# Optimization experiments

Hardware: AMD Instinct MI355X
Metric: run time of the kernel (lower is better)

Reference implementation:

```python
import jax, jax.numpy as jnp
import numpy as np

B, S, D, F = 8, 2048, 256, 8

def setup_inputs() -> dict:
    key = jax.random.key(0)
    ks = jax.random.split(key, 7)
    hidden_states = jax.random.normal(ks[0], (B, S, D), dtype=jnp.float32)
    # flat indices into zero-prepended [1 + B*S, D] token table; 0 = padding row
    select_idx = jax.random.randint(ks[1], (B, S, F), 0, B * S + 1, dtype=jnp.int32)
    word_mask = jax.random.randint(ks[2], (B, S), 0, 2, dtype=jnp.int32)
    W1 = jax.random.normal(ks[3], (D, D), dtype=jnp.float32) * (1.0 / np.sqrt(D))
    b1 = jax.random.normal(ks[4], (D,), dtype=jnp.float32) * 0.02
    w2 = jax.random.normal(ks[5], (D,), dtype=jnp.float32) * (1.0 / np.sqrt(D))
    b2 = jax.random.normal(ks[6], (1,), dtype=jnp.float32) * 0.02
    return {"hidden_states": hidden_states, "select_idx": select_idx,
            "word_mask": word_mask, "W1": W1, "b1": b1, "w2": w2, "b2": b2}

def reference(hidden_states, select_idx, word_mask, W1, b1, w2, b2):
    b, s, d = hidden_states.shape
    h = jnp.tanh(hidden_states.reshape(-1, d) @ W1.T + b1)          # [B*S, D]
    h = jnp.concatenate([jnp.zeros((1, d), h.dtype), h], axis=0)    # zero padding row at index 0
    g = h[select_idx.reshape(-1)]                                    # gather: [B*S*F, D]
    g = g.reshape(b * s, -1, d).max(axis=1)                          # AdaptiveMaxPool1d(1) over word occurrences
    scores = (g @ w2 + b2[0]).reshape(b, s)                          # w2 linear -> [B, S]
    neg = -10000.0 * (1.0 - word_mask.astype(jnp.float32))
    return scores.astype(jnp.float32) + neg
```

## Files before the change

### kernel.cpp

```cpp
#include <hip/hip_runtime.h>
#include <hip/hip_bf16.h>
#include <math.h>

#define BB 8
#define SS 2048
#define DD 256
#define FF 8
#define NTOK (BB*SS)

typedef __bf16 bf16x8 __attribute__((ext_vector_type(8)));
typedef float  f32x4  __attribute__((ext_vector_type(4)));
typedef float  f32x2  __attribute__((ext_vector_type(2)));

#define BM 128
#define BN 64
#define BK 32
#define NSTEP (DD/BK)
#define XS 40

__device__ __forceinline__ float fast_tanh(float x) {
    float e = __expf(2.0f * x);
    return 1.0f - 2.0f * __builtin_amdgcn_rcpf(e + 1.0f);
}

__device__ __forceinline__ unsigned pack2_bf16(float a, float b) {
    return (__float_as_uint(a) >> 16) | (__float_as_uint(b) & 0xFFFF0000u);
}

__device__ __forceinline__ unsigned char f32_to_fp8(float v) {
    return (unsigned char)(__builtin_amdgcn_cvt_pk_fp8_f32(v, v, 0, false) & 0xFF);
}

__global__ __launch_bounds__(512, 4) void gemm_tanh_kernel(
    const float* __restrict__ x, const float* __restrict__ W1,
    const float* __restrict__ b1, unsigned char* __restrict__ table)
{
    __shared__ __align__(16) unsigned short xs[2][BM * XS];
    __shared__ __align__(16) unsigned short wsb[2][BN * XS];

    const int tid  = threadIdx.x;
    const int bx   = blockIdx.x;
    const int tok0 = (bx >> 2) * BM;
    const int n0   = (bx & 3) * BN;

    if (bx == 0 && tid < 64) ((unsigned int*)table)[tid] = 0u;

    const int wave = tid >> 6, lane = tid & 63;
    const int wm = wave >> 1;
    const int wn = wave & 1;
    const int lr = lane & 15;
    const int kg = lane >> 4;

    f32x4 xr[2], wr;

    auto load_chunk = [&](int k0) {
        #pragma unroll
        for (int rep = 0; rep < 2; ++rep) {
            int slot = rep * 512 + tid;
            int row = slot >> 3, kc = slot & 7;
            xr[rep] = *(const f32x4*)&x[(size_t)(tok0 + row) * DD + k0 + kc * 4];
        }
        {
            int row = tid >> 3, kc = tid & 7;
            wr = *(const f32x4*)&W1[(size_t)(n0 + row) * DD + k0 + kc * 4];
        }
    };
    auto store_lds = [&](int buf) {
        #pragma unroll
        for (int rep = 0; rep < 2; ++rep) {
            int slot = rep * 512 + tid;
            int row = slot >> 3, kc = slot & 7;
            uint2 p;
            p.x = pack2_bf16(xr[rep].x, xr[rep].y);
            p.y = pack2_bf16(xr[rep].z, xr[rep].w);
            *(uint2*)&xs[buf][row * XS + kc * 4] = p;
        }
        {
            int row = tid >> 3, kc = tid & 7;
            uint2 p;
            p.x = pack2_bf16(wr.x, wr.y);
            p.y = pack2_bf16(wr.z, wr.w);
            *(uint2*)&wsb[buf][row * XS + kc * 4] = p;
        }
    };

    f32x4 acc[2][2];
    #pragma unroll
    for (int mf = 0; mf < 2; ++mf)
        #pragma unroll
        for (int nf = 0; nf < 2; ++nf)
            acc[mf][nf] = (f32x4){0.f, 0.f, 0.f, 0.f};

    load_chunk(0);
    for (int s = 0; s < NSTEP; ++s) {
        const int buf = s & 1;
        store_lds(buf);
        __syncthreads();
        if (s + 1 < NSTEP) load_chunk((s + 1) * BK);

        bf16x8 af[2], bfr[2];
        #pragma unroll
        for (int mf = 0; mf < 2; ++mf) {
            int m = wm * 32 + mf * 16 + lr;
            af[mf] = *(const bf16x8*)&xs[buf][m * XS + kg * 8];
        }
        #pragma unroll
        for (int nf = 0; nf < 2; ++nf) {
            int n = wn * 32 + nf * 16 + lr;
            bfr[nf] = *(const bf16x8*)&wsb[buf][n * XS + kg * 8];
        }
        #pragma unroll
        for (int mf = 0; mf < 2; ++mf)
            #pragma unroll
            for (int nf = 0; nf < 2; ++nf)
                acc[mf][nf] = __builtin_amdgcn_mfma_f32_16x16x32_bf16(
                    af[mf], bfr[nf], acc[mf][nf], 0, 0, 0);
        __syncthreads();
    }

    float bj[2];
    #pragma unroll
    for (int nf = 0; nf < 2; ++nf) bj[nf] = b1[n0 + wn * 32 + nf * 16 + lr];

    #pragma unroll
    for (int mf = 0; mf < 2; ++mf) {
        #pragma unroll
        for (int r = 0; r < 4; ++r) {
            int m = tok0 + wm * 32 + mf * 16 + kg * 4 + r;
            size_t rowbase = (size_t)(1 + m) * DD;
            #pragma unroll
            for (int nf = 0; nf < 2; ++nf) {
                float v = fast_tanh(acc[mf][nf][r] + bj[nf]);
                table[rowbase + n0 + wn * 32 + nf * 16 + lr] = f32_to_fp8(v);
            }
        }
    }
}

__global__ __launch_bounds__(256) void gather_score_kernel(
    const unsigned char* __restrict__ table,
    const int* __restrict__ select_idx,
    const int* __restrict__ word_mask,
    const float* __restrict__ w2,
    const float* __restrict__ b2,
    float* __restrict__ out)
{
    const int tid  = threadIdx.x;
    const int lane = tid & 63;
    const int wv   = tid >> 6;
    const int i    = blockIdx.x * 4 + wv;
    const int half = lane >> 5;
    const int c    = lane & 31;
    const int d0   = c * 8;

    const int4* sp = (const int4*)(select_idx + (size_t)i * FF);
    int4 q0 = sp[0], q1 = sp[1];
    int rows[4];
    rows[0] = half ? q0.y : q0.x;
    rows[1] = half ? q0.w : q0.z;
    rows[2] = half ? q1.y : q1.x;
    rows[3] = half ? q1.w : q1.z;

    float m[8];
    #pragma unroll
    for (int j = 0; j < 8; ++j) m[j] = -INFINITY;

    #pragma unroll
    for (int it = 0; it < 4; ++it) {
        uint2 u = *(const uint2*)(table + (size_t)rows[it] * DD + d0);
        f32x2 a0 = __builtin_amdgcn_cvt_pk_f32_fp8(u.x, false);
        f32x2 a1 = __builtin_amdgcn_cvt_pk_f32_fp8(u.x, true);
        f32x2 a2 = __builtin_amdgcn_cvt_pk_f32_fp8(u.y, false);
        f32x2 a3 = __builtin_amdgcn_cvt_pk_f32_fp8(u.y, true);
        m[0] = fmaxf(m[0], a0.x); m[1] = fmaxf(m[1], a0.y);
        m[2] = fmaxf(m[2], a1.x); m[3] = fmaxf(m[3], a1.y);
        m[4] = fmaxf(m[4], a2.x); m[5] = fmaxf(m[5], a2.y);
        m[6] = fmaxf(m[6], a3.x); m[7] = fmaxf(m[7], a3.y);
    }

    #pragma unroll
    for (int j = 0; j < 8; ++j) m[j] = fmaxf(m[j], __shfl_xor(m[j], 32));

    f32x4 wa = *(const f32x4*)&w2[d0];
    f32x4 wb = *(const f32x4*)&w2[d0 + 4];
    float p = m[0] * wa.x + m[1] * wa.y + m[2] * wa.z + m[3] * wa.w
            + m[4] * wb.x + m[5] * wb.y + m[6] * wb.z + m[7] * wb.w;

    #pragma unroll
    for (int off = 16; off; off >>= 1) p += __shfl_xor(p, off);

    if (lane == 0) {
        float neg = word_mask[i] ? 0.f : -10000.f;
        out[i] = p + b2[0] + neg;
    }
}

extern "C" void kernel_launch(void* const* d_in, const int* in_sizes, int n_in,
                              void* d_out, int out_size, void* d_ws, size_t ws_size,
                              hipStream_t stream) {
    const float* hs    = (const float*)d_in[0];
    const int*   sidx  = (const int*)  d_in[1];
    const int*   wmask = (const int*)  d_in[2];
    const float* W1    = (const float*)d_in[3];
    const float* b1    = (const float*)d_in[4];
    const float* w2    = (const float*)d_in[5];
    const float* b2    = (const float*)d_in[6];
    float* out = (float*)d_out;

    unsigned char* table = (unsigned char*)d_ws;

    gemm_tanh_kernel<<<(NTOK / BM) * (DD / BN), 512, 0, stream>>>(hs, W1, b1, table);
    gather_score_kernel<<<NTOK / 4, 256, 0, stream>>>(table, sidx, wmask, w2, b2, out);
}
```

Before: 91.90 us.

## Double K tile, prefetch into alternate LDS buffer, stage output through LDS

```diff
diff --git a/kernel.cpp b/kernel.cpp
--- a/kernel.cpp
+++ b/kernel.cpp
@@ -14,9 +14,9 @@
 
 #define BM 128
 #define BN 64
-#define BK 32
+#define BK 64
 #define NSTEP (DD/BK)
-#define XS 40
+#define XS 72
 
 __device__ __forceinline__ float fast_tanh(float x) {
     float e = __expf(2.0f * x);
@@ -40,8 +40,10 @@
 
     const int tid  = threadIdx.x;
     const int bx   = blockIdx.x;
-    const int tok0 = (bx >> 2) * BM;
-    const int n0   = (bx & 3) * BN;
+    const int tokgrp = bx & 127;
+    const int nblk   = bx >> 7;
+    const int tok0 = tokgrp * BM;
+    const int n0   = nblk * BN;
 
     if (bx == 0 && tid < 64) ((unsigned int*)table)[tid] = 0u;
 
@@ -51,35 +53,39 @@
     const int lr = lane & 15;
     const int kg = lane >> 4;
 
-    f32x4 xr[2], wr;
+    f32x4 xr[4], wr[2];
 
     auto load_chunk = [&](int k0) {
         #pragma unroll
+        for (int rep = 0; rep < 4; ++rep) {
+            int slot = rep * 512 + tid;
+            int row = slot >> 4, kc = slot & 15;
+            xr[rep] = *(const f32x4*)&x[(size_t)(tok0 + row) * DD + k0 + kc * 4];
+        }
+        #pragma unroll
         for (int rep = 0; rep < 2; ++rep) {
             int slot = rep * 512 + tid;
-            int row = slot >> 3, kc = slot & 7;
-            xr[rep] = *(const f32x4*)&x[(size_t)(tok0 + row) * DD + k0 + kc * 4];
-        }
-        {
-            int row = tid >> 3, kc = tid & 7;
-            wr = *(const f32x4*)&W1[(size_t)(n0 + row) * DD + k0 + kc * 4];
+            int row = slot >> 4, kc = slot & 15;
+            wr[rep] = *(const f32x4*)&W1[(size_t)(n0 + row) * DD + k0 + kc * 4];
         }
     };
     auto store_lds = [&](int buf) {
         #pragma unroll
-        for (int rep = 0; rep < 2; ++rep) {
-            int slot = rep * 512 + tid;
-            int row = slot >> 3, kc = slot & 7;
+        for (int rep = 0; rep < 4; ++rep) {
+            int slot = rep * 512 + tid;
+            int row = slot >> 4, kc = slot & 15;
             uint2 p;
             p.x = pack2_bf16(xr[rep].x, xr[rep].y);
             p.y = pack2_bf16(xr[rep].z, xr[rep].w);
             *(uint2*)&xs[buf][row * XS + kc * 4] = p;
         }
-        {
-            int row = tid >> 3, kc = tid & 7;
+        #pragma unroll
+        for (int rep = 0; rep < 2; ++rep) {
+            int slot = rep * 512 + tid;
+            int row = slot >> 4, kc = slot & 15;
             uint2 p;
-            p.x = pack2_bf16(wr.x, wr.y);
-            p.y = pack2_bf16(wr.z, wr.w);
+            p.x = pack2_bf16(wr[rep].x, wr[rep].y);
+            p.y = pack2_bf16(wr[rep].z, wr[rep].w);
             *(uint2*)&wsb[buf][row * XS + kc * 4] = p;
         }
     };
@@ -92,48 +98,63 @@
             acc[mf][nf] = (f32x4){0.f, 0.f, 0.f, 0.f};
 
     load_chunk(0);
+    store_lds(0);
+
     for (int s = 0; s < NSTEP; ++s) {
+        __syncthreads();
         const int buf = s & 1;
-        store_lds(buf);
-        __syncthreads();
         if (s + 1 < NSTEP) load_chunk((s + 1) * BK);
 
-        bf16x8 af[2], bfr[2];
-        #pragma unroll
-        for (int mf = 0; mf < 2; ++mf) {
-            int m = wm * 32 + mf * 16 + lr;
-            af[mf] = *(const bf16x8*)&xs[buf][m * XS + kg * 8];
-        }
-        #pragma unroll
-        for (int nf = 0; nf < 2; ++nf) {
-            int n = wn * 32 + nf * 16 + lr;
-            bfr[nf] = *(const bf16x8*)&wsb[buf][n * XS + kg * 8];
-        }
-        #pragma unroll
-        for (int mf = 0; mf < 2; ++mf)
-            #pragma unroll
-            for (int nf = 0; nf < 2; ++nf)
-                acc[mf][nf] = __builtin_amdgcn_mfma_f32_16x16x32_bf16(
-                    af[mf], bfr[nf], acc[mf][nf], 0, 0, 0);
-        __syncthreads();
+        bf16x8 af[2][2], bfr[2][2];
+        #pragma unroll
+        for (int c = 0; c < 2; ++c) {
+            #pragma unroll
+            for (int mf = 0; mf < 2; ++mf) {
+                int m = wm * 32 + mf * 16 + lr;
+                af[c][mf] = *(const bf16x8*)&xs[buf][m * XS + c * 32 + kg * 8];
+            }
+            #pragma unroll
+            for (int nf = 0; nf < 2; ++nf) {
+                int n = wn * 32 + nf * 16 + lr;
+                bfr[c][nf] = *(const bf16x8*)&wsb[buf][n * XS + c * 32 + kg * 8];
+            }
+        }
+        if (s + 1 < NSTEP) store_lds(buf ^ 1);
+
+        #pragma unroll
+        for (int c = 0; c < 2; ++c)
+            #pragma unroll
+            for (int mf = 0; mf < 2; ++mf)
+                #pragma unroll
+                for (int nf = 0; nf < 2; ++nf)
+                    acc[mf][nf] = __builtin_amdgcn_mfma_f32_16x16x32_bf16(
+                        af[c][mf], bfr[c][nf], acc[mf][nf], 0, 0, 0);
     }
 
     float bj[2];
     #pragma unroll
     for (int nf = 0; nf < 2; ++nf) bj[nf] = b1[n0 + wn * 32 + nf * 16 + lr];
 
+    __syncthreads();
+    unsigned char* sc = (unsigned char*)&xs[0][0];
     #pragma unroll
     for (int mf = 0; mf < 2; ++mf) {
         #pragma unroll
         for (int r = 0; r < 4; ++r) {
-            int m = tok0 + wm * 32 + mf * 16 + kg * 4 + r;
-            size_t rowbase = (size_t)(1 + m) * DD;
+            int m = wm * 32 + mf * 16 + kg * 4 + r;
             #pragma unroll
             for (int nf = 0; nf < 2; ++nf) {
                 float v = fast_tanh(acc[mf][nf][r] + bj[nf]);
-                table[rowbase + n0 + wn * 32 + nf * 16 + lr] = f32_to_fp8(v);
+                sc[m * 80 + wn * 32 + nf * 16 + lr] = f32_to_fp8(v);
             }
         }
+    }
+    __syncthreads();
+    {
+        int row = tid >> 2;
+        int off = (tid & 3) * 16;
+        uint4 v = *(const uint4*)&sc[row * 80 + off];
+        *(uint4*)&table[(size_t)(1 + tok0 + row) * DD + n0 + off] = v;
     }
 }
 
```

New measurement: 85.75 us, median of 2. 1.07x faster.
